# Kernel optimization log

Measured on AMD Instinct MI355X. Metric: run time of the kernel, lower is better.

Reference implementation:

```python
import jax, jax.numpy as jnp
import numpy as np

B, F, C, D = 4, 60082, 14695, 256
KN, KH = 64, 128


def _leaky(x):
    return jnp.where(x >= 0, x, 0.01 * x)  # nn.LeakyReLU default slope


def setup_inputs() -> dict:
    key = jax.random.key(0)
    ks = jax.random.split(key, 20)
    d = {}
    d["company_emb"] = jax.random.normal(ks[0], (B, D), jnp.float32)
    d["field_emb"] = jax.random.normal(ks[1], (F, D), jnp.float32)
    d["raw_field_embed"] = jax.random.normal(ks[2], (F, D), jnp.float32)
    d["comp_table"] = jax.random.normal(ks[3], (C, D), jnp.float32)
    d["field_table"] = jax.random.normal(ks[4], (F, D), jnp.float32)
    d["W_proj"] = jax.random.normal(ks[5], (D, D), jnp.float32) / np.sqrt(D)
    d["b_proj"] = jnp.zeros((D,), jnp.float32)
    d["theta"] = jax.random.uniform(ks[6], (C, 1), jnp.float32)
    d["alpha_fields"] = jax.random.uniform(ks[7], (F, 1), jnp.float32)
    d["w_ff"] = jax.random.normal(ks[8], (D,), jnp.float32) / np.sqrt(D)
    d["b_ff"] = jnp.zeros((), jnp.float32)
    d["w_fc"] = jax.random.normal(ks[9], (D,), jnp.float32) / np.sqrt(D)
    d["b_fc"] = jnp.zeros((), jnp.float32)
    d["W1"] = jax.random.normal(ks[10], (D, D // 2), jnp.float32) / np.sqrt(D)
    d["b1"] = jnp.zeros((D // 2,), jnp.float32)
    d["W2"] = jax.random.normal(ks[11], (D // 2, D), jnp.float32) / np.sqrt(D // 2)
    d["b2"] = jnp.zeros((D,), jnp.float32)
    d["now_nodes"] = jax.random.randint(ks[12], (B, KN), 0, F, dtype=jnp.int32)
    d["his_nodes"] = jax.random.randint(ks[13], (B, KH), 0, F, dtype=jnp.int32)
    d["com_id"] = jax.random.randint(ks[14], (B,), 0, C, dtype=jnp.int32)
    return d


def reference(company_emb, field_emb, raw_field_embed, comp_table, field_table,
              W_proj, b_proj, theta, alpha_fields, w_ff, b_ff, w_fc, b_fc,
              W1, b1, W2, b2, now_nodes, his_nodes, com_id):
    # company memory/static mix: (B, D)
    th = theta[com_id]  # (B, 1)
    company_mem = (1.0 - th) * company_emb + th * comp_table[com_id]
    # (dropout is identity in eval mode)

    # shared projected field table: (F, D)
    embed_base = field_table @ W_proj + b_proj

    bidx = jnp.arange(B)[:, None]
    # beta mask: 1 at now + his indices per batch element
    beta = (jnp.zeros((B, F), jnp.float32)
            .at[bidx, now_nodes].set(1.0)
            .at[bidx, his_nodes].set(1.0))
    alpha = alpha_fields[:, 0]  # (F,)

    # (B, F, D) scaled base embedding
    embed = (1.0 - beta * alpha[None, :])[..., None] * embed_base[None]

    # now-node additive update (gather-then-set, matching torch advanced assignment)
    now_proj = field_emb[now_nodes]  # (B, KN, D)
    embed = embed.at[bidx, now_nodes].set(
        embed[bidx, now_nodes] + alpha_fields[now_nodes] * now_proj)

    # his-node MLP update: Linear -> LeakyReLU -> Linear on raw field memory
    h = _leaky(raw_field_embed[his_nodes] @ W1 + b1) @ W2 + b2  # (B, KH, D)
    embed = embed.at[bidx, his_nodes].set(
        embed[bidx, his_nodes] + alpha_fields[his_nodes] * h)

    fields_out = embed @ w_ff + b_ff        # (B, F)
    company_out = company_mem @ w_fc + b_fc  # (B,)
    return fields_out + company_out[:, None]
```

## Files before the change

### kernel.cpp

```cpp
#include <hip/hip_runtime.h>

#define Dc 256
#define Bc 4
#define Fc 60082
#define KNc 64
#define KHc 128


__device__ __forceinline__ float wave_reduce_sum_bfly(float v) {
    #pragma unroll
    for (int off = 32; off > 0; off >>= 1)
        v += __shfl_xor(v, off, 64);
    return v;
}

__global__ void k_pre(const float* __restrict__ company_emb,
                      const float* __restrict__ comp_table,
                      const float* __restrict__ W_proj,
                      const float* __restrict__ b_proj,
                      const float* __restrict__ theta,
                      const float* __restrict__ w_ff,
                      const float* __restrict__ b_ff,
                      const float* __restrict__ w_fc,
                      const float* __restrict__ b_fc,
                      const float* __restrict__ W2,
                      const float* __restrict__ b2,
                      const int* __restrict__ com_id,
                      float* __restrict__ ws)
{
    int gw = (blockIdx.x * blockDim.x + threadIdx.x) >> 6;
    int lane = threadIdx.x & 63;
    if (gw >= 390) return;

    const float4* wf4 = (const float4*)w_ff;
    float val = 0.f;
    float addend = 0.f;
    float* dst;

    if (gw < 256) {
        float4 a = ((const float4*)(W_proj + (size_t)gw * Dc))[lane];
        float4 b = wf4[lane];
        val = a.x*b.x + a.y*b.y + a.z*b.z + a.w*b.w;
        dst = ws + gw;
    } else if (gw < 384) {
        int j = gw - 256;
        float4 a = ((const float4*)(W2 + (size_t)j * Dc))[lane];
        float4 b = wf4[lane];
        val = a.x*b.x + a.y*b.y + a.z*b.z + a.w*b.w;
        dst = ws + 256 + j;
    } else if (gw < 388) {
        int b_ = gw - 384;
        int cid = com_id[b_];
        float th = theta[cid];
        float4 x = ((const float4*)(company_emb + (size_t)b_ * Dc))[lane];
        float4 y = ((const float4*)(comp_table + (size_t)cid * Dc))[lane];
        float4 w = ((const float4*)w_fc)[lane];
        float4 m;
        m.x = (1.f - th) * x.x + th * y.x;
        m.y = (1.f - th) * x.y + th * y.y;
        m.z = (1.f - th) * x.z + th * y.z;
        m.w = (1.f - th) * x.w + th * y.w;
        val = m.x*w.x + m.y*w.y + m.z*w.z + m.w*w.w;
        addend = b_fc[0] + b_ff[0];
        dst = ws + 384 + b_;
    } else if (gw == 388) {
        float4 a = ((const float4*)b2)[lane];
        float4 b = wf4[lane];
        val = a.x*b.x + a.y*b.y + a.z*b.z + a.w*b.w;
        dst = ws + 388;
    } else {
        float4 a = ((const float4*)b_proj)[lane];
        float4 b = wf4[lane];
        val = a.x*b.x + a.y*b.y + a.z*b.z + a.w*b.w;
        dst = ws + 389;
    }
    val = wave_reduce_sum_bfly(val);
    if (lane == 0) *dst = val + addend;
}

#define RPW 8
__global__ void k_s(const float* __restrict__ field_table,
                    const float* __restrict__ ws,
                    float* __restrict__ s,
                    float* __restrict__ out)
{
    int gw = (blockIdx.x * blockDim.x + threadIdx.x) >> 6;
    int lane = threadIdx.x & 63;
    int f0 = gw * RPW;
    if (f0 >= Fc) return;

    int sub = lane >> 4;
    int c   = lane & 15;

    const float4* u4 = (const float4*)ws;
    float4 b0 = u4[c];
    float4 b1 = u4[c + 16];
    float4 b2 = u4[c + 32];
    float4 b3 = u4[c + 48];
    float c0 = ws[389];

    float sums[2];
    #pragma unroll
    for (int pass = 0; pass < 2; ++pass) {
        int f = f0 + pass * 4 + sub;
        float4 a0, a1, a2, a3;
        if (f < Fc) {
            const float4* row = (const float4*)(field_table + (size_t)f * Dc);
            a0 = row[c];
            a1 = row[c + 16];
            a2 = row[c + 32];
            a3 = row[c + 48];
        } else {
            a0 = a1 = a2 = a3 = make_float4(0.f, 0.f, 0.f, 0.f);
        }
        float acc = a0.x*b0.x + a0.y*b0.y + a0.z*b0.z + a0.w*b0.w
                  + a1.x*b1.x + a1.y*b1.y + a1.z*b1.z + a1.w*b1.w
                  + a2.x*b2.x + a2.y*b2.y + a2.z*b2.z + a2.w*b2.w
                  + a3.x*b3.x + a3.y*b3.y + a3.z*b3.z + a3.w*b3.w;
        acc += __shfl_xor(acc, 1, 64);
        acc += __shfl_xor(acc, 2, 64);
        acc += __shfl_xor(acc, 4, 64);
        acc += __shfl_xor(acc, 8, 64);
        sums[pass] = acc;
    }

    #pragma unroll
    for (int pass = 0; pass < 2; ++pass) {
        int f = f0 + pass * 4 + sub;
        if (f >= Fc) continue;
        float sv = sums[pass] + c0;
        if (c < Bc) {
            out[(size_t)c * Fc + f] = sv + ws[384 + c];
        } else if (c == Bc) {
            s[f] = sv;
        }
    }
}

__global__ void k_fix(const float* __restrict__ field_emb,
                      const float* __restrict__ raw_field_embed,
                      const float* __restrict__ alpha_fields,
                      const float* __restrict__ w_ff,
                      const float* __restrict__ W1,
                      const float* __restrict__ b1,
                      const float* __restrict__ ws,
                      const float* __restrict__ s,
                      const int* __restrict__ now_nodes,
                      const int* __restrict__ his_nodes,
                      float* __restrict__ out)
{
    const float* v2     = ws + 256;
    const float* constb = ws + 384;
    const float* scal   = ws + 388;

    const int NPB = KNc + KHc;
    int gw = (blockIdx.x * blockDim.x + threadIdx.x) >> 6;
    int lane = threadIdx.x & 63;
    if (gw >= Bc * NPB) return;
    int b = gw / NPB;
    int k = gw - b * NPB;
    int f = (k < KNc) ? now_nodes[b * KNc + k]
                      : his_nodes[b * KHc + (k - KNc)];

    int nn = now_nodes[b * KNc + lane];
    bool in_now = __any(nn == f);
    int h0 = his_nodes[b * KHc + lane];
    int h1 = his_nodes[b * KHc + 64 + lane];
    bool in_his = __any((h0 == f) || (h1 == f));

    float alpha = alpha_fields[f];
    float val = (1.f - alpha) * s[f] + constb[b];

    if (in_now) {
        float4 a  = ((const float4*)(field_emb + (size_t)f * Dc))[lane];
        float4 ww = ((const float4*)w_ff)[lane];
        float acc = a.x*ww.x + a.y*ww.y + a.z*ww.z + a.w*ww.w;
        acc = wave_reduce_sum_bfly(acc);
        val += alpha * acc;
    }
    if (in_his) {
        float acc0 = 0.f, acc1 = 0.f;
        const float4* raw4 = (const float4*)(raw_field_embed + (size_t)f * Dc);
        #pragma unroll 2
        for (int d4 = 0; d4 < Dc / 4; ++d4) {
            float4 r4 = raw4[d4];
            const float* base = W1 + d4 * 4 * 128;
            acc0 += r4.x * base[lane]       + r4.y * base[128 + lane]
                  + r4.z * base[256 + lane] + r4.w * base[384 + lane];
            acc1 += r4.x * base[64 + lane]      + r4.y * base[128 + 64 + lane]
                  + r4.z * base[256 + 64 + lane] + r4.w * base[384 + 64 + lane];
        }
        float g0 = acc0 + b1[lane];
        float g1 = acc1 + b1[64 + lane];
        g0 = (g0 >= 0.f) ? g0 : 0.01f * g0;
        g1 = (g1 >= 0.f) ? g1 : 0.01f * g1;
        float p = g0 * v2[lane] + g1 * v2[64 + lane];
        p = wave_reduce_sum_bfly(p);
        val += alpha * (p + scal[0]);
    }
    if (lane == 0) out[(size_t)b * Fc + f] = val;
}

extern "C" void kernel_launch(void* const* d_in, const int* in_sizes, int n_in,
                              void* d_out, int out_size, void* d_ws, size_t ws_size,
                              hipStream_t stream) {
    const float* company_emb     = (const float*)d_in[0];
    const float* field_emb       = (const float*)d_in[1];
    const float* raw_field_embed = (const float*)d_in[2];
    const float* comp_table      = (const float*)d_in[3];
    const float* field_table     = (const float*)d_in[4];
    const float* W_proj          = (const float*)d_in[5];
    const float* b_proj          = (const float*)d_in[6];
    const float* theta           = (const float*)d_in[7];
    const float* alpha_fields    = (const float*)d_in[8];
    const float* w_ff            = (const float*)d_in[9];
    const float* b_ff            = (const float*)d_in[10];
    const float* w_fc            = (const float*)d_in[11];
    const float* b_fc            = (const float*)d_in[12];
    const float* W1              = (const float*)d_in[13];
    const float* b1              = (const float*)d_in[14];
    const float* W2              = (const float*)d_in[15];
    const float* b2              = (const float*)d_in[16];
    const int*   now_nodes       = (const int*)d_in[17];
    const int*   his_nodes       = (const int*)d_in[18];
    const int*   com_id          = (const int*)d_in[19];

    float* ws  = (float*)d_ws;
    float* s   = ws + 512;
    float* out = (float*)d_out;

    k_pre<<<(390 + 3) / 4, 256, 0, stream>>>(company_emb, comp_table, W_proj, b_proj,
                                             theta, w_ff, b_ff, w_fc, b_fc, W2, b2,
                                             com_id, ws);

    int waves = (Fc + RPW - 1) / RPW;
    k_s<<<(waves + 3) / 4, 256, 0, stream>>>(field_table, ws, s, out);

    int fix_blocks = (Bc * (KNc + KHc)) / 4;
    k_fix<<<fix_blocks, 256, 0, stream>>>(field_emb, raw_field_embed, alpha_fields,
                                          w_ff, W1, b1, ws, s,
                                          now_nodes, his_nodes, out);
}
```

Measured before the change: 220.4 us.

## Fuse node fix-up into streaming pass and move gathers into precompute kernel

Goes from three launches to two. The now-node dot products and his-node MLP hidden activations are computed in the first kernel alongside the weight-vector folds. The streaming kernel builds a per-block shared-memory mask of touched fields and applies the corrections inline. This removes the separate fix-up launch, the intermediate s array write, and the dependent serial stage. The cost is a per-block scan of all 768 indices into shared memory with atomics, plus extra branching in the hot streaming kernel.

```diff
diff --git a/kernel.cpp b/kernel.cpp
--- a/kernel.cpp
+++ b/kernel.cpp
@@ -6,6 +6,13 @@
 #define KNc 64
 #define KHc 128
 
+#define WS_U   0
+#define WS_V2  256
+#define WS_CB  384
+#define WS_C2  388
+#define WS_C0  389
+#define WS_NT  390
+#define WS_G   768
 
 __device__ __forceinline__ float wave_reduce_sum_bfly(float v) {
     #pragma unroll
@@ -14,171 +21,83 @@
     return v;
 }
 
-__global__ void k_pre(const float* __restrict__ company_emb,
-                      const float* __restrict__ comp_table,
-                      const float* __restrict__ W_proj,
-                      const float* __restrict__ b_proj,
-                      const float* __restrict__ theta,
-                      const float* __restrict__ w_ff,
-                      const float* __restrict__ b_ff,
-                      const float* __restrict__ w_fc,
-                      const float* __restrict__ b_fc,
-                      const float* __restrict__ W2,
-                      const float* __restrict__ b2,
-                      const int* __restrict__ com_id,
-                      float* __restrict__ ws)
+__global__ void k1(const float* __restrict__ company_emb,
+                   const float* __restrict__ field_emb,
+                   const float* __restrict__ raw_field_embed,
+                   const float* __restrict__ comp_table,
+                   const float* __restrict__ W_proj,
+                   const float* __restrict__ b_proj,
+                   const float* __restrict__ theta,
+                   const float* __restrict__ w_ff,
+                   const float* __restrict__ b_ff,
+                   const float* __restrict__ w_fc,
+                   const float* __restrict__ b_fc,
+                   const float* __restrict__ W1,
+                   const float* __restrict__ b1,
+                   const float* __restrict__ W2,
+                   const float* __restrict__ b2,
+                   const int* __restrict__ now_nodes,
+                   const int* __restrict__ his_nodes,
+                   const int* __restrict__ com_id,
+                   float* __restrict__ ws)
 {
     int gw = (blockIdx.x * blockDim.x + threadIdx.x) >> 6;
     int lane = threadIdx.x & 63;
-    if (gw >= 390) return;
-
     const float4* wf4 = (const float4*)w_ff;
-    float val = 0.f;
-    float addend = 0.f;
-    float* dst;
-
-    if (gw < 256) {
-        float4 a = ((const float4*)(W_proj + (size_t)gw * Dc))[lane];
+
+    if (gw < 390) {
+        float val = 0.f, addend = 0.f;
+        float* dst;
+        if (gw < 256) {
+            float4 a = ((const float4*)(W_proj + (size_t)gw * Dc))[lane];
+            float4 b = wf4[lane];
+            val = a.x*b.x + a.y*b.y + a.z*b.z + a.w*b.w;
+            dst = ws + WS_U + gw;
+        } else if (gw < 384) {
+            int j = gw - 256;
+            float4 a = ((const float4*)(W2 + (size_t)j * Dc))[lane];
+            float4 b = wf4[lane];
+            val = a.x*b.x + a.y*b.y + a.z*b.z + a.w*b.w;
+            dst = ws + WS_V2 + j;
+        } else if (gw < 388) {
+            int b_ = gw - 384;
+            int cid = com_id[b_];
+            float th = theta[cid];
+            float4 x = ((const float4*)(company_emb + (size_t)b_ * Dc))[lane];
+            float4 y = ((const float4*)(comp_table + (size_t)cid * Dc))[lane];
+            float4 w = ((const float4*)w_fc)[lane];
+            float4 m;
+            m.x = (1.f - th) * x.x + th * y.x;
+            m.y = (1.f - th) * x.y + th * y.y;
+            m.z = (1.f - th) * x.z + th * y.z;
+            m.w = (1.f - th) * x.w + th * y.w;
+            val = m.x*w.x + m.y*w.y + m.z*w.z + m.w*w.w;
+            addend = b_fc[0] + b_ff[0];
+            dst = ws + WS_CB + b_;
+        } else if (gw == 388) {
+            float4 a = ((const float4*)b2)[lane];
+            float4 b = wf4[lane];
+            val = a.x*b.x + a.y*b.y + a.z*b.z + a.w*b.w;
+            dst = ws + WS_C2;
+        } else {
+            float4 a = ((const float4*)b_proj)[lane];
+            float4 b = wf4[lane];
+            val = a.x*b.x + a.y*b.y + a.z*b.z + a.w*b.w;
+            dst = ws + WS_C0;
+        }
+        val = wave_reduce_sum_bfly(val);
+        if (lane == 0) *dst = val + addend;
+    } else if (gw < 646) {
+        int slot = gw - 390;
+        int f = now_nodes[slot];
+        float4 a = ((const float4*)(field_emb + (size_t)f * Dc))[lane];
         float4 b = wf4[lane];
-        val = a.x*b.x + a.y*b.y + a.z*b.z + a.w*b.w;
-        dst = ws + gw;
-    } else if (gw < 384) {
-        int j = gw - 256;
-        float4 a = ((const float4*)(W2 + (size_t)j * Dc))[lane];
-        float4 b = wf4[lane];
-        val = a.x*b.x + a.y*b.y + a.z*b.z + a.w*b.w;
-        dst = ws + 256 + j;
-    } else if (gw < 388) {
-        int b_ = gw - 384;
-        int cid = com_id[b_];
-        float th = theta[cid];
-        float4 x = ((const float4*)(company_emb + (size_t)b_ * Dc))[lane];
-        float4 y = ((const float4*)(comp_table + (size_t)cid * Dc))[lane];
-        float4 w = ((const float4*)w_fc)[lane];
-        float4 m;
-        m.x = (1.f - th) * x.x + th * y.x;
-        m.y = (1.f - th) * x.y + th * y.y;
-        m.z = (1.f - th) * x.z + th * y.z;
-        m.w = (1.f - th) * x.w + th * y.w;
-        val = m.x*w.x + m.y*w.y + m.z*w.z + m.w*w.w;
-        addend = b_fc[0] + b_ff[0];
-        dst = ws + 384 + b_;
-    } else if (gw == 388) {
-        float4 a = ((const float4*)b2)[lane];
-        float4 b = wf4[lane];
-        val = a.x*b.x + a.y*b.y + a.z*b.z + a.w*b.w;
-        dst = ws + 388;
-    } else {
-        float4 a = ((const float4*)b_proj)[lane];
-        float4 b = wf4[lane];
-        val = a.x*b.x + a.y*b.y + a.z*b.z + a.w*b.w;
-        dst = ws + 389;
-    }
-    val = wave_reduce_sum_bfly(val);
-    if (lane == 0) *dst = val + addend;
-}
-
-#define RPW 8
-__global__ void k_s(const float* __restrict__ field_table,
-                    const float* __restrict__ ws,
-                    float* __restrict__ s,
-                    float* __restrict__ out)
-{
-    int gw = (blockIdx.x * blockDim.x + threadIdx.x) >> 6;
-    int lane = threadIdx.x & 63;
-    int f0 = gw * RPW;
-    if (f0 >= Fc) return;
-
-    int sub = lane >> 4;
-    int c   = lane & 15;
-
-    const float4* u4 = (const float4*)ws;
-    float4 b0 = u4[c];
-    float4 b1 = u4[c + 16];
-    float4 b2 = u4[c + 32];
-    float4 b3 = u4[c + 48];
-    float c0 = ws[389];
-
-    float sums[2];
-    #pragma unroll
-    for (int pass = 0; pass < 2; ++pass) {
-        int f = f0 + pass * 4 + sub;
-        float4 a0, a1, a2, a3;
-        if (f < Fc) {
-            const float4* row = (const float4*)(field_table + (size_t)f * Dc);
-            a0 = row[c];
-            a1 = row[c + 16];
-            a2 = row[c + 32];
-            a3 = row[c + 48];
-        } else {
-            a0 = a1 = a2 = a3 = make_float4(0.f, 0.f, 0.f, 0.f);
-        }
-        float acc = a0.x*b0.x + a0.y*b0.y + a0.z*b0.z + a0.w*b0.w
-                  + a1.x*b1.x + a1.y*b1.y + a1.z*b1.z + a1.w*b1.w
-                  + a2.x*b2.x + a2.y*b2.y + a2.z*b2.z + a2.w*b2.w
-                  + a3.x*b3.x + a3.y*b3.y + a3.z*b3.z + a3.w*b3.w;
-        acc += __shfl_xor(acc, 1, 64);
-        acc += __shfl_xor(acc, 2, 64);
-        acc += __shfl_xor(acc, 4, 64);
-        acc += __shfl_xor(acc, 8, 64);
-        sums[pass] = acc;
-    }
-
-    #pragma unroll
-    for (int pass = 0; pass < 2; ++pass) {
-        int f = f0 + pass * 4 + sub;
-        if (f >= Fc) continue;
-        float sv = sums[pass] + c0;
-        if (c < Bc) {
-            out[(size_t)c * Fc + f] = sv + ws[384 + c];
-        } else if (c == Bc) {
-            s[f] = sv;
-        }
-    }
-}
-
-__global__ void k_fix(const float* __restrict__ field_emb,
-                      const float* __restrict__ raw_field_embed,
-                      const float* __restrict__ alpha_fields,
-                      const float* __restrict__ w_ff,
-                      const float* __restrict__ W1,
-                      const float* __restrict__ b1,
-                      const float* __restrict__ ws,
-                      const float* __restrict__ s,
-                      const int* __restrict__ now_nodes,
-                      const int* __restrict__ his_nodes,
-                      float* __restrict__ out)
-{
-    const float* v2     = ws + 256;
-    const float* constb = ws + 384;
-    const float* scal   = ws + 388;
-
-    const int NPB = KNc + KHc;
-    int gw = (blockIdx.x * blockDim.x + threadIdx.x) >> 6;
-    int lane = threadIdx.x & 63;
-    if (gw >= Bc * NPB) return;
-    int b = gw / NPB;
-    int k = gw - b * NPB;
-    int f = (k < KNc) ? now_nodes[b * KNc + k]
-                      : his_nodes[b * KHc + (k - KNc)];
-
-    int nn = now_nodes[b * KNc + lane];
-    bool in_now = __any(nn == f);
-    int h0 = his_nodes[b * KHc + lane];
-    int h1 = his_nodes[b * KHc + 64 + lane];
-    bool in_his = __any((h0 == f) || (h1 == f));
-
-    float alpha = alpha_fields[f];
-    float val = (1.f - alpha) * s[f] + constb[b];
-
-    if (in_now) {
-        float4 a  = ((const float4*)(field_emb + (size_t)f * Dc))[lane];
-        float4 ww = ((const float4*)w_ff)[lane];
-        float acc = a.x*ww.x + a.y*ww.y + a.z*ww.z + a.w*ww.w;
-        acc = wave_reduce_sum_bfly(acc);
-        val += alpha * acc;
-    }
-    if (in_his) {
+        float val = a.x*b.x + a.y*b.y + a.z*b.z + a.w*b.w;
+        val = wave_reduce_sum_bfly(val);
+        if (lane == 0) ws[WS_NT + slot] = val;
+    } else if (gw < 1158) {
+        int slot = gw - 646;
+        int f = his_nodes[slot];
         float acc0 = 0.f, acc1 = 0.f;
         const float4* raw4 = (const float4*)(raw_field_embed + (size_t)f * Dc);
         #pragma unroll 2
@@ -187,18 +106,131 @@
             const float* base = W1 + d4 * 4 * 128;
             acc0 += r4.x * base[lane]       + r4.y * base[128 + lane]
                   + r4.z * base[256 + lane] + r4.w * base[384 + lane];
-            acc1 += r4.x * base[64 + lane]      + r4.y * base[128 + 64 + lane]
+            acc1 += r4.x * base[64 + lane]       + r4.y * base[128 + 64 + lane]
                   + r4.z * base[256 + 64 + lane] + r4.w * base[384 + 64 + lane];
         }
         float g0 = acc0 + b1[lane];
         float g1 = acc1 + b1[64 + lane];
         g0 = (g0 >= 0.f) ? g0 : 0.01f * g0;
         g1 = (g1 >= 0.f) ? g1 : 0.01f * g1;
-        float p = g0 * v2[lane] + g1 * v2[64 + lane];
-        p = wave_reduce_sum_bfly(p);
-        val += alpha * (p + scal[0]);
-    }
-    if (lane == 0) out[(size_t)b * Fc + f] = val;
+        float* gr = ws + WS_G + (size_t)slot * 128;
+        gr[lane]      = g0;
+        gr[64 + lane] = g1;
+    }
+}
+
+#define RPW 8
+#define RPB 32
+
+__global__ void k2(const float* __restrict__ field_table,
+                   const float* __restrict__ alpha_fields,
+                   const int* __restrict__ now_nodes,
+                   const int* __restrict__ his_nodes,
+                   const float* __restrict__ ws,
+                   float* __restrict__ out)
+{
+    __shared__ int   mark[RPB];
+    __shared__ short know_[RPB][Bc];
+    __shared__ short khis_[RPB][Bc];
+
+    int tid  = threadIdx.x;
+    int lane = tid & 63;
+    int wloc = tid >> 6;
+    int f0b  = blockIdx.x * RPB;
+
+    if (tid < RPB) mark[tid] = 0;
+    __syncthreads();
+
+    #pragma unroll
+    for (int e = tid; e < Bc * (KNc + KHc); e += 256) {
+        int b = e / (KNc + KHc);
+        int j = e - b * (KNc + KHc);
+        int f, bit; short kk;
+        if (j < KNc) { f = now_nodes[b * KNc + j];         bit = 1 << b;       kk = (short)j; }
+        else         { f = his_nodes[b * KHc + (j - KNc)]; bit = 1 << (4 + b); kk = (short)(j - KNc); }
+        int rel = f - f0b;
+        if (rel >= 0 && rel < RPB) {
+            atomicOr(&mark[rel], bit);
+            if (j < KNc) know_[rel][b] = kk; else khis_[rel][b] = kk;
+        }
+    }
+    __syncthreads();
+
+    int sub = lane >> 4;
+    int c   = lane & 15;
+    const float4* u4 = (const float4*)(ws + WS_U);
+    float4 ub0 = u4[c], ub1 = u4[c + 16], ub2 = u4[c + 32], ub3 = u4[c + 48];
+    float c0 = ws[WS_C0];
+    float cb = (c < Bc) ? ws[WS_CB + c] : 0.f;
+    int fbase = f0b + wloc * RPW;
+
+    float sums[2];
+    #pragma unroll
+    for (int pass = 0; pass < 2; ++pass) {
+        int f = fbase + pass * 4 + sub;
+        float4 a0, a1, a2, a3;
+        if (f < Fc) {
+            const float4* row = (const float4*)(field_table + (size_t)f * Dc);
+            a0 = row[c]; a1 = row[c + 16]; a2 = row[c + 32]; a3 = row[c + 48];
+        } else {
+            a0 = a1 = a2 = a3 = make_float4(0.f, 0.f, 0.f, 0.f);
+        }
+        float acc = a0.x*ub0.x + a0.y*ub0.y + a0.z*ub0.z + a0.w*ub0.w
+                  + a1.x*ub1.x + a1.y*ub1.y + a1.z*ub1.z + a1.w*ub1.w
+                  + a2.x*ub2.x + a2.y*ub2.y + a2.z*ub2.z + a2.w*ub2.w
+                  + a3.x*ub3.x + a3.y*ub3.y + a3.z*ub3.z + a3.w*ub3.w;
+        acc += __shfl_xor(acc, 1, 64);
+        acc += __shfl_xor(acc, 2, 64);
+        acc += __shfl_xor(acc, 4, 64);
+        acc += __shfl_xor(acc, 8, 64);
+        sums[pass] = acc;
+    }
+
+    #pragma unroll
+    for (int pass = 0; pass < 2; ++pass) {
+        int r = pass * 4 + sub;
+        int f = fbase + r;
+        if (f < Fc && c < Bc) {
+            int m = mark[wloc * RPW + r];
+            if (!(m & (0x11 << c)))
+                out[(size_t)c * Fc + f] = sums[pass] + c0 + cb;
+        }
+    }
+
+    bool any = false;
+    #pragma unroll
+    for (int r = 0; r < RPW; ++r) any = any || (mark[wloc * RPW + r] != 0);
+    if (!any) return;
+
+    float v2l = ws[WS_V2 + lane];
+    float v2h = ws[WS_V2 + 64 + lane];
+    float c2  = ws[WS_C2];
+    for (int r = 0; r < RPW; ++r) {
+        int m = mark[wloc * RPW + r];
+        if (!m) continue;
+        int f = fbase + r;
+        if (f >= Fc) continue;
+        float alpha = alpha_fields[f];
+        float s0 = __shfl(sums[0], (r & 3) << 4, 64);
+        float s1 = __shfl(sums[1], (r & 3) << 4, 64);
+        float sv = ((r >> 2) ? s1 : s0) + c0;
+        #pragma unroll
+        for (int b = 0; b < Bc; ++b) {
+            int mb = (m >> b) & 0x11;
+            if (!mb) continue;
+            float val = (1.f - alpha) * sv + ws[WS_CB + b];
+            if (mb & 1)
+                val += alpha * ws[WS_NT + b * KNc + know_[wloc * RPW + r][b]];
+            if (mb & 0x10) {
+                const float* gr = ws + WS_G
+                                + (size_t)(b * KHc + khis_[wloc * RPW + r][b]) * 128;
+                float p = gr[lane] * v2l + gr[64 + lane] * v2h;
+                p = wave_reduce_sum_bfly(p);
+                val += alpha * (p + c2);
+            }
+            if (lane == 0) out[(size_t)b * Fc + f] = val;
+        }
+    }
 }
 
 extern "C" void kernel_launch(void* const* d_in, const int* in_sizes, int n_in,
@@ -226,18 +258,13 @@
     const int*   com_id          = (const int*)d_in[19];
 
     float* ws  = (float*)d_ws;
-    float* s   = ws + 512;
     float* out = (float*)d_out;
 
-    k_pre<<<(390 + 3) / 4, 256, 0, stream>>>(company_emb, comp_table, W_proj, b_proj,
-                                             theta, w_ff, b_ff, w_fc, b_fc, W2, b2,
-                                             com_id, ws);
-
-    int waves = (Fc + RPW - 1) / RPW;
-    k_s<<<(waves + 3) / 4, 256, 0, stream>>>(field_table, ws, s, out);
-
-    int fix_blocks = (Bc * (KNc + KHc)) / 4;
-    k_fix<<<fix_blocks, 256, 0, stream>>>(field_emb, raw_field_embed, alpha_fields,
-                                          w_ff, W1, b1, ws, s,
-                                          now_nodes, his_nodes, out);
-}
+    k1<<<(1158 + 3) / 4, 256, 0, stream>>>(company_emb, field_emb, raw_field_embed,
+                                           comp_table, W_proj, b_proj, theta,
+                                           w_ff, b_ff, w_fc, b_fc, W1, b1, W2, b2,
+                                           now_nodes, his_nodes, com_id, ws);
+
+    k2<<<(Fc + RPB - 1) / RPB, 256, 0, stream>>>(field_table, alpha_fields,
+                                                 now_nodes, his_nodes, ws, out);
+}
```

Result: no change. 218.3 us (-0.9%).
